# Performance work log

Hardware: AMD Instinct MI355X
Metric: run time of the kernel (lower is better)

## Reference

```python
import jax, jax.numpy as jnp
import numpy as np

HID = 256
STYLE_DIM = 64
NUM_STYLES = 8
IN_DIM = 3 + STYLE_DIM


def setup_inputs() -> dict:
    key = jax.random.key(0)
    ks = jax.random.split(key, 12)
    B, H, W = 2, 512, 512
    rgb = jax.random.uniform(ks[0], (B, 3, H, W), dtype=jnp.float32)
    style_idx = jax.random.randint(ks[1], (B,), 0, NUM_STYLES, dtype=jnp.int32)
    # style embedding table (torch init: normal std=0.01)
    emb_table = 0.01 * jax.random.normal(ks[2], (NUM_STYLES, STYLE_DIM), dtype=jnp.float32)
    # kaiming-normal (fan_in, relu gain sqrt(2)) weights stored as [in, out]
    def kaiming(k, fan_in, fan_out):
        std = np.sqrt(2.0 / fan_in)
        return std * jax.random.normal(k, (fan_in, fan_out), dtype=jnp.float32)
    W0 = kaiming(ks[3], IN_DIM, HID); b0 = jnp.zeros((HID,), jnp.float32)
    W1 = kaiming(ks[4], HID, HID);    b1 = jnp.zeros((HID,), jnp.float32)
    W2 = kaiming(ks[5], HID, HID);    b2 = jnp.zeros((HID,), jnp.float32)
    W3 = kaiming(ks[6], HID, 3);      b3 = jnp.zeros((3,), jnp.float32)
    return {"rgb": rgb, "style_idx": style_idx, "emb_table": emb_table,
            "W0": W0, "b0": b0, "W1": W1, "b1": b1,
            "W2": W2, "b2": b2, "W3": W3, "b3": b3}


def reference(rgb, style_idx, emb_table, W0, b0, W1, b1, W2, b2, W3, b3):
    B, C, H, W_ = rgb.shape  # CHW image input
    # [B,3,H,W] -> [B*H*W, 3]
    rgb_flat = jnp.transpose(rgb, (0, 2, 3, 1)).reshape(-1, 3)
    # style embedding lookup, broadcast per pixel
    emb = emb_table[style_idx]                              # [B, style_dim]
    emb = jnp.broadcast_to(emb[:, None, :], (B, H * W_, STYLE_DIM)).reshape(-1, STYLE_DIM)
    x = jnp.concatenate([rgb_flat, emb], axis=-1)           # [N, 67]
    gelu = lambda t: jax.nn.gelu(t, approximate=False)      # torch nn.GELU default (erf)
    x = gelu(x @ W0 + b0)
    x = gelu(x @ W1 + b1)
    x = gelu(x @ W2 + b2)
    out_flat = jax.nn.sigmoid(x @ W3 + b3)                  # [N, 3]
    out = out_flat.reshape(B, H, W_, 3).transpose(0, 3, 1, 2)
    return out
```

## Files before the change

kernel.cpp:

```cpp
#include <hip/hip_runtime.h>

#define HW  (512*512)

typedef _Float16 half8  __attribute__((__vector_size__(16)));
typedef _Float16 half4  __attribute__((__vector_size__(8)));
typedef _Float16 half2_t __attribute__((__vector_size__(4)));
typedef float    floatx4 __attribute__((__vector_size__(16)));

__device__ __forceinline__ float gelu_f(float x){
    float x2 = x * x;
    float q  = __builtin_fmaf(x2, -0.1029432f, -2.3022079f);
    float e  = __builtin_amdgcn_exp2f(x * q);
    return x * __builtin_amdgcn_rcpf(1.0f + e);
}

__device__ __forceinline__ float sigmoid_f(float x){
    float e = __builtin_amdgcn_exp2f(-1.44269504f * x);
    return __builtin_amdgcn_rcpf(1.0f + e);
}


__global__ void prep_all(const float* __restrict__ W1, const float* __restrict__ W2,
                         const float* __restrict__ W3, const float* __restrict__ emb,
                         const int* __restrict__ sidx, const float* __restrict__ W0,
                         const float* __restrict__ b0,
                         _Float16* __restrict__ wp, float* __restrict__ c0){
    __shared__ float ld[32][68];
    int blk = blockIdx.x;
    int tid = threadIdx.x;
    if (blk < 64){
        int mat = blk >> 5;
        int g   = blk & 31;
        int ks  = g >> 2;
        int ntq = g & 3;
        const float* W = mat ? W2 : W1;
        int row = tid >> 3;
        int c8  = (tid & 7) * 8;
        const float* src = &W[(ks*32 + row)*256 + ntq*64 + c8];
        *(floatx4*)&ld[row][c8]     = *(const floatx4*)src;
        *(floatx4*)&ld[row][c8 + 4] = *(const floatx4*)(src + 4);
        __syncthreads();
        int lane = tid & 63;
        int nt_l = tid >> 6;
        half8 h;
        #pragma unroll
        for (int j = 0; j < 8; j++)
            h[j] = (_Float16)ld[(lane >> 4)*8 + j][nt_l*16 + (lane & 15)];
        _Float16* dst = wp + mat*65536 + (ks*16 + ntq*4 + nt_l)*512 + lane*8;
        *(half8*)dst = h;
    } else if (blk < 80){
        int i    = (blk - 64)*256 + tid;
        int j    = i & 7;
        int lane = (i >> 3) & 63;
        int ks   = i >> 9;
        int k = ks*32 + ((lane >> 4) << 3) + j;
        int n = lane & 15;
        wp[131072 + i] = (_Float16)((n < 3) ? W3[k*3 + n] : 0.0f);
    } else {
        int b = blk - 80;
        int s = sidx[b];
        float acc = b0[tid];
        #pragma unroll 8
        for (int d = 0; d < 64; d++)
            acc = fmaf(emb[s*64 + d], W0[(3 + d)*256 + tid], acc);
        c0[b*256 + tid] = acc;
    }
}

__global__ __launch_bounds__(256, 4)
void nilut_main(const float* __restrict__ rgb,
                const float* __restrict__ W0,
                const float* __restrict__ b1v,
                const float* __restrict__ b2v,
                const float* __restrict__ b3v,
                const _Float16* __restrict__ wp,
                const float* __restrict__ c0,
                float* __restrict__ out){
    __shared__ __align__(16) _Float16 act[64 * 256];
    __shared__ __align__(16) float    w0s[1024];
    __shared__ __align__(16) float    rgbs[192];

    const int tid = threadIdx.x;
    const int wg  = blockIdx.x;
    const int pixbase = wg * 64;
    const int b   = pixbase >> 18;
    const int hw0 = pixbase & (HW - 1);

    #pragma unroll
    for (int r = 0; r < 4; r++){
        int q = r*256 + tid;
        w0s[q] = (q < 768) ? W0[q] : c0[b*256 + (q - 768)];
    }
    if (tid < 192){
        int c = tid >> 6, row = tid & 63;
        rgbs[tid] = rgb[b*3*HW + c*HW + hw0 + row];
    }
    __syncthreads();

    {
        int ng = tid & 31;
        int rg = tid >> 5;
        floatx4 cw[4][2];
        #pragma unroll
        for (int p = 0; p < 4; p++){
            cw[p][0] = *(const floatx4*)&w0s[p*256 + ng*8];
            cw[p][1] = *(const floatx4*)&w0s[p*256 + ng*8 + 4];
        }
        #pragma unroll
        for (int hf = 0; hf < 2; hf++){
            floatx4 rv[3];
            #pragma unroll
            for (int c = 0; c < 3; c++)
                rv[c] = *(const floatx4*)&rgbs[c*64 + rg*8 + hf*4];
            #pragma unroll
            for (int r4 = 0; r4 < 4; r4++){
                int row = rg*8 + hf*4 + r4;
                float rr = rv[0][r4], gg = rv[1][r4], bb = rv[2][r4];
                half8 v;
                #pragma unroll
                for (int j = 0; j < 8; j++){
                    int hi = j >> 2, lo = j & 3;
                    float z = fmaf(rr, cw[0][hi][lo],
                              fmaf(gg, cw[1][hi][lo],
                              fmaf(bb, cw[2][hi][lo], cw[3][hi][lo])));
                    v[j] = (_Float16)gelu_f(z);
                }
                *(half8*)&act[row*256 + ((ng ^ (row & 7)) << 3)] = v;
            }
        }
    }
    __syncthreads();

    const int lane = tid & 63;
    const int wv   = tid >> 6;
    const int ln15 = lane & 15;
    const int quad = lane >> 4;
    const int qr   = quad * 4;
    const int sx   = ln15 & 7;
    const int qx8  = (quad ^ (sx & 3)) * 8;
    const int kb32 = ((sx >> 2) & 1) << 5;

    int pbq[4];
    #pragma unroll
    for (int pt = 0; pt < 4; pt++)
        pbq[pt] = (pt*16 + ln15)*256 + qx8;

    const int qh = quad >> 1, qs = (quad & 1) * 4;
    int eb[4];
    #pragma unroll
    for (int pt = 0; pt < 4; pt++)
        eb[pt] = (pt*16 + ln15)*256 + qs;

    const _Float16* wl  = wp;
    const float* bias   = b1v;
    #pragma unroll 1
    for (int L = 0; L < 2; L++){
        floatx4 acc[4][4];
        #pragma unroll
        for (int mtl = 0; mtl < 4; mtl++){
            floatx4 bv = *(const floatx4*)&bias[(wv*4 + mtl)*16 + qr];
            #pragma unroll
            for (int pt = 0; pt < 4; pt++)
                acc[pt][mtl] = bv;
        }

        const half8* wp8 = (const half8*)wl;
        #pragma unroll 2
        for (int ks = 0; ks < 8; ks++){
            int t = (ks << 5) ^ kb32;
            half8 bfr[4];
            #pragma unroll
            for (int pt = 0; pt < 4; pt++)
                bfr[pt] = *(const half8*)&act[pbq[pt] + t];
            #pragma unroll
            for (int mtl = 0; mtl < 4; mtl++){
                half8 af = wp8[(ks*16 + wv*4 + mtl)*64 + lane];
                #pragma unroll
                for (int pt = 0; pt < 4; pt++)
                    acc[pt][mtl] = __builtin_amdgcn_mfma_f32_16x16x32_f16(af, bfr[pt], acc[pt][mtl], 0, 0, 0);
            }
        }
        __syncthreads();
        #pragma unroll
        for (int mtl = 0; mtl < 4; mtl++){
            int cx = (((wv*4 + mtl)*2 + qh) ^ sx) << 3;
            #pragma unroll
            for (int pt = 0; pt < 4; pt++){
                floatx4 v = acc[pt][mtl];
                half2_t g01 = __builtin_amdgcn_cvt_pkrtz(gelu_f(v[0]), gelu_f(v[1]));
                half2_t g23 = __builtin_amdgcn_cvt_pkrtz(gelu_f(v[2]), gelu_f(v[3]));
                half4 h;
                h[0] = g01[0]; h[1] = g01[1]; h[2] = g23[0]; h[3] = g23[1];
                *(half4*)&act[eb[pt] + cx] = h;
            }
        }
        __syncthreads();
        wl = wp + 65536;
        bias = b2v;
    }

    {
        const half8* wp8 = (const half8*)(wp + 131072);
        floatx4 ac = (floatx4){0.f,0.f,0.f,0.f};
        int pb = (wv*16 + ln15)*256 + qx8;
        #pragma unroll
        for (int ks = 0; ks < 8; ks++){
            half8 bfr = *(const half8*)&act[pb + ((ks << 5) ^ kb32)];
            half8 af  = wp8[ks*64 + lane];
            ac = __builtin_amdgcn_mfma_f32_16x16x32_f16(af, bfr, ac, 0, 0, 0);
        }
        if (quad == 0){
            #pragma unroll
            for (int r = 0; r < 3; r++)
                w0s[r*64 + wv*16 + ln15] = sigmoid_f(ac[r] + b3v[r]);
        }
        __syncthreads();
        if (tid < 48){
            int c  = tid >> 4;
            int i2 = tid & 15;
            float4* dst = (float4*)(out + (b*3 + c)*HW + hw0);
            dst[i2] = ((float4*)(w0s + c*64))[i2];
        }
    }
}

extern "C" void kernel_launch(void* const* d_in, const int* in_sizes, int n_in,
                              void* d_out, int out_size, void* d_ws, size_t ws_size,
                              hipStream_t stream){
    const float* rgb = (const float*)d_in[0];
    const int*  sidx = (const int*) d_in[1];
    const float* emb = (const float*)d_in[2];
    const float* W0  = (const float*)d_in[3];
    const float* b0  = (const float*)d_in[4];
    const float* W1  = (const float*)d_in[5];
    const float* b1  = (const float*)d_in[6];
    const float* W2  = (const float*)d_in[7];
    const float* b2  = (const float*)d_in[8];
    const float* W3  = (const float*)d_in[9];
    const float* b3  = (const float*)d_in[10];
    float* out = (float*)d_out;

    _Float16* wp = (_Float16*)d_ws;
    float*    c0 = (float*)((char*)d_ws + 270336);

    int n_pix = in_sizes[0] / 3;
    prep_all<<<82, 256, 0, stream>>>(W1, W2, W3, emb, sidx, W0, b0, wp, c0);
    nilut_main<<<n_pix / 64, 256, 0, stream>>>(rgb, W0, b1, b2, b3, wp, c0, out);
}
```

Baseline: 266.2 us.

## Split workgroup pixels into two halves and interleave MFMA with GELU epilogues

Each 64-pixel workgroup is split into two 32-pixel halves with separate LDS activation buffers. The layer stages are software-pipelined so one half's matrix multiply runs alongside the other half's GELU epilogue or first-layer compute, letting MFMA and VALU work overlap. The cost is more barriers, doubled weight fragment loads from global/L2 per pixel (each weight fragment now feeds two MFMAs instead of four), and two accumulator sets alive at once. The final layer uses only two waves per half.

```diff
diff --git a/kernel.cpp b/kernel.cpp
--- a/kernel.cpp
+++ b/kernel.cpp
@@ -67,6 +67,12 @@
     }
 }
 
+struct Acc { floatx4 a[2][4]; };
+
+__device__ __forceinline__ floatx4 mfma16(half8 a, half8 b, floatx4 c){
+    return __builtin_amdgcn_mfma_f32_16x16x32_f16(a, b, c, 0, 0, 0);
+}
+
 __global__ __launch_bounds__(256, 4)
 void nilut_main(const float* __restrict__ rgb,
                 const float* __restrict__ W0,
@@ -76,7 +82,7 @@
                 const _Float16* __restrict__ wp,
                 const float* __restrict__ c0,
                 float* __restrict__ out){
-    __shared__ __align__(16) _Float16 act[64 * 256];
+    __shared__ __align__(16) _Float16 act[2][32 * 256];
     __shared__ __align__(16) float    w0s[1024];
     __shared__ __align__(16) float    rgbs[192];
 
@@ -94,40 +100,6 @@
     if (tid < 192){
         int c = tid >> 6, row = tid & 63;
         rgbs[tid] = rgb[b*3*HW + c*HW + hw0 + row];
-    }
-    __syncthreads();
-
-    {
-        int ng = tid & 31;
-        int rg = tid >> 5;
-        floatx4 cw[4][2];
-        #pragma unroll
-        for (int p = 0; p < 4; p++){
-            cw[p][0] = *(const floatx4*)&w0s[p*256 + ng*8];
-            cw[p][1] = *(const floatx4*)&w0s[p*256 + ng*8 + 4];
-        }
-        #pragma unroll
-        for (int hf = 0; hf < 2; hf++){
-            floatx4 rv[3];
-            #pragma unroll
-            for (int c = 0; c < 3; c++)
-                rv[c] = *(const floatx4*)&rgbs[c*64 + rg*8 + hf*4];
-            #pragma unroll
-            for (int r4 = 0; r4 < 4; r4++){
-                int row = rg*8 + hf*4 + r4;
-                float rr = rv[0][r4], gg = rv[1][r4], bb = rv[2][r4];
-                half8 v;
-                #pragma unroll
-                for (int j = 0; j < 8; j++){
-                    int hi = j >> 2, lo = j & 3;
-                    float z = fmaf(rr, cw[0][hi][lo],
-                              fmaf(gg, cw[1][hi][lo],
-                              fmaf(bb, cw[2][hi][lo], cw[3][hi][lo])));
-                    v[j] = (_Float16)gelu_f(z);
-                }
-                *(half8*)&act[row*256 + ((ng ^ (row & 7)) << 3)] = v;
-            }
-        }
     }
     __syncthreads();
 
@@ -139,89 +111,121 @@
     const int sx   = ln15 & 7;
     const int qx8  = (quad ^ (sx & 3)) * 8;
     const int kb32 = ((sx >> 2) & 1) << 5;
-
-    int pbq[4];
+    const int qh   = quad >> 1, qs = (quad & 1) * 4;
+    const int pb0  = ln15*256 + qx8,  pb1 = (16 + ln15)*256 + qx8;
+    const int eb0  = ln15*256 + qs,   eb1 = (16 + ln15)*256 + qs;
+    const int ng   = tid & 31, rg = tid >> 5;
+
+    const half8* wp1 = (const half8*)wp;
+    const half8* wp2 = (const half8*)(wp + 65536);
+    const half8* wp3 = (const half8*)(wp + 131072);
+
+    floatx4 cw[4][2];
     #pragma unroll
-    for (int pt = 0; pt < 4; pt++)
-        pbq[pt] = (pt*16 + ln15)*256 + qx8;
-
-    const int qh = quad >> 1, qs = (quad & 1) * 4;
-    int eb[4];
-    #pragma unroll
-    for (int pt = 0; pt < 4; pt++)
-        eb[pt] = (pt*16 + ln15)*256 + qs;
-
-    const _Float16* wl  = wp;
-    const float* bias   = b1v;
-    #pragma unroll 1
-    for (int L = 0; L < 2; L++){
-        floatx4 acc[4][4];
+    for (int p = 0; p < 4; p++){
+        cw[p][0] = *(const floatx4*)&w0s[p*256 + ng*8];
+        cw[p][1] = *(const floatx4*)&w0s[p*256 + ng*8 + 4];
+    }
+
+    Acc accA, accB;
+    floatx4 accfA = (floatx4){0.f,0.f,0.f,0.f};
+    floatx4 accfB = (floatx4){0.f,0.f,0.f,0.f};
+
+    auto L0 = [&](int s){
+        floatx4 rv[3];
+        #pragma unroll
+        for (int c = 0; c < 3; c++)
+            rv[c] = *(const floatx4*)&rgbs[c*64 + s*32 + rg*4];
+        #pragma unroll
+        for (int r4 = 0; r4 < 4; r4++){
+            int px = rg*4 + r4;
+            float rr = rv[0][r4], gg = rv[1][r4], bb = rv[2][r4];
+            half8 v;
+            #pragma unroll
+            for (int j = 0; j < 8; j++){
+                int hi = j >> 2, lo = j & 3;
+                float z = fmaf(rr, cw[0][hi][lo],
+                          fmaf(gg, cw[1][hi][lo],
+                          fmaf(bb, cw[2][hi][lo], cw[3][hi][lo])));
+                v[j] = (_Float16)gelu_f(z);
+            }
+            *(half8*)&act[s][px*256 + ((ng ^ (px & 7)) << 3)] = v;
+        }
+    };
+
+    auto KL = [&](int s, const half8* w8, const float* bias, Acc& A){
         #pragma unroll
         for (int mtl = 0; mtl < 4; mtl++){
             floatx4 bv = *(const floatx4*)&bias[(wv*4 + mtl)*16 + qr];
-            #pragma unroll
-            for (int pt = 0; pt < 4; pt++)
-                acc[pt][mtl] = bv;
-        }
-
-        const half8* wp8 = (const half8*)wl;
+            A.a[0][mtl] = bv; A.a[1][mtl] = bv;
+        }
         #pragma unroll 2
         for (int ks = 0; ks < 8; ks++){
             int t = (ks << 5) ^ kb32;
-            half8 bfr[4];
-            #pragma unroll
-            for (int pt = 0; pt < 4; pt++)
-                bfr[pt] = *(const half8*)&act[pbq[pt] + t];
+            half8 bf0 = *(const half8*)&act[s][pb0 + t];
+            half8 bf1 = *(const half8*)&act[s][pb1 + t];
             #pragma unroll
             for (int mtl = 0; mtl < 4; mtl++){
-                half8 af = wp8[(ks*16 + wv*4 + mtl)*64 + lane];
-                #pragma unroll
-                for (int pt = 0; pt < 4; pt++)
-                    acc[pt][mtl] = __builtin_amdgcn_mfma_f32_16x16x32_f16(af, bfr[pt], acc[pt][mtl], 0, 0, 0);
+                half8 af = w8[(ks*16 + wv*4 + mtl)*64 + lane];
+                A.a[0][mtl] = mfma16(af, bf0, A.a[0][mtl]);
+                A.a[1][mtl] = mfma16(af, bf1, A.a[1][mtl]);
             }
         }
-        __syncthreads();
+    };
+
+    auto EP = [&](int s, Acc& A){
         #pragma unroll
         for (int mtl = 0; mtl < 4; mtl++){
             int cx = (((wv*4 + mtl)*2 + qh) ^ sx) << 3;
             #pragma unroll
-            for (int pt = 0; pt < 4; pt++){
-                floatx4 v = acc[pt][mtl];
+            for (int pt = 0; pt < 2; pt++){
+                floatx4 v = A.a[pt][mtl];
                 half2_t g01 = __builtin_amdgcn_cvt_pkrtz(gelu_f(v[0]), gelu_f(v[1]));
                 half2_t g23 = __builtin_amdgcn_cvt_pkrtz(gelu_f(v[2]), gelu_f(v[3]));
                 half4 h;
                 h[0] = g01[0]; h[1] = g01[1]; h[2] = g23[0]; h[3] = g23[1];
-                *(half4*)&act[eb[pt] + cx] = h;
+                *(half4*)&act[s][(pt ? eb1 : eb0) + cx] = h;
             }
         }
-        __syncthreads();
-        wl = wp + 65536;
-        bias = b2v;
-    }
-
-    {
-        const half8* wp8 = (const half8*)(wp + 131072);
-        floatx4 ac = (floatx4){0.f,0.f,0.f,0.f};
-        int pb = (wv*16 + ln15)*256 + qx8;
-        #pragma unroll
-        for (int ks = 0; ks < 8; ks++){
-            half8 bfr = *(const half8*)&act[pb + ((ks << 5) ^ kb32)];
-            half8 af  = wp8[ks*64 + lane];
-            ac = __builtin_amdgcn_mfma_f32_16x16x32_f16(af, bfr, ac, 0, 0, 0);
-        }
-        if (quad == 0){
+    };
+
+    auto K3 = [&](int s, floatx4& af){
+        if (wv < 2){
+            floatx4 a = (floatx4){0.f,0.f,0.f,0.f};
+            int pb = (wv*16 + ln15)*256 + qx8;
+            #pragma unroll
+            for (int ks = 0; ks < 8; ks++)
+                a = mfma16(wp3[ks*64 + lane],
+                           *(const half8*)&act[s][pb + ((ks << 5) ^ kb32)], a);
+            af = a;
+        }
+    };
+
+    auto OUTSIG = [&](int s, floatx4 af){
+        if (wv < 2 && quad == 0){
             #pragma unroll
             for (int r = 0; r < 3; r++)
-                w0s[r*64 + wv*16 + ln15] = sigmoid_f(ac[r] + b3v[r]);
-        }
-        __syncthreads();
-        if (tid < 48){
-            int c  = tid >> 4;
-            int i2 = tid & 15;
-            float4* dst = (float4*)(out + (b*3 + c)*HW + hw0);
-            dst[i2] = ((float4*)(w0s + c*64))[i2];
-        }
-    }
+                w0s[s*96 + r*32 + wv*16 + ln15] = sigmoid_f(af[r] + b3v[r]);
+        }
+    };
+
+    auto STORE = [&](int s){
+        if (tid < 24){
+            int c = tid >> 3, i = tid & 7;
+            float4* dst = (float4*)(out + (b*3 + c)*HW + hw0 + s*32);
+            dst[i] = ((float4*)(w0s + s*96 + c*32))[i];
+        }
+    };
+
+    L0(0);                         __syncthreads();
+    KL(0, wp1, b1v, accA); L0(1);  __syncthreads();
+    EP(0, accA); KL(1, wp1, b1v, accB); __syncthreads();
+    KL(0, wp2, b2v, accA); EP(1, accB); __syncthreads();
+    EP(0, accA); KL(1, wp2, b2v, accB); __syncthreads();
+    K3(0, accfA); EP(1, accB);     __syncthreads();
+    OUTSIG(0, accfA); K3(1, accfB); __syncthreads();
+    STORE(0); OUTSIG(1, accfB);    __syncthreads();
+    STORE(1);
 }
 
 extern "C" void kernel_launch(void* const* d_in, const int* in_sizes, int n_in,
```

Result: slower. 304.8 us (+14.5%).
